# Kernel tuning notes

Measured on AMD Instinct MI355X. Metric: run time of the kernel, lower is better.

Reference implementation:

```python
import jax, jax.numpy as jnp
import numpy as np

N, K = 50000, 16
IN_FEATS, HIDDEN, T2V = 128, 128, 64


def time2vec(t, w0, b0, W, B):
    # t: [..., 1] -> [..., T2V]; linear term + sin periodic terms
    lin = t * w0 + b0                      # [..., 1]
    per = jnp.sin(t * W + B)               # [..., T2V-1]
    return jnp.concatenate([lin, per], axis=-1)


def setup_inputs() -> dict:
    key = jax.random.key(0)
    ks = jax.random.split(key, 12)
    s = 0.05
    return {
        "x": jax.random.normal(ks[0], (N, IN_FEATS), jnp.float32),
        "ts": jax.random.uniform(ks[1], (N, K), jnp.float32),
        "idx": jax.random.randint(ks[2], (N, K), 0, N),
        "t2v_w0": jax.random.normal(ks[3], (1,), jnp.float32),
        "t2v_b0": jax.random.normal(ks[4], (1,), jnp.float32),
        "t2v_W": jax.random.normal(ks[5], (T2V - 1,), jnp.float32),
        "t2v_B": jax.random.normal(ks[6], (T2V - 1,), jnp.float32),
        "Wq": jax.random.normal(ks[7], (IN_FEATS + T2V, HIDDEN), jnp.float32) * s,
        "Wk": jax.random.normal(ks[8], (IN_FEATS + T2V, HIDDEN), jnp.float32) * s,
        "Wv": jax.random.normal(ks[9], (IN_FEATS + T2V, HIDDEN), jnp.float32) * s,
        "Wo": jax.random.normal(ks[10], (HIDDEN, HIDDEN), jnp.float32) * s,
        "bo": jnp.zeros((HIDDEN,), jnp.float32),
    }


def reference(x, ts, idx, t2v_w0, t2v_b0, t2v_W, t2v_B, Wq, Wk, Wv, Wo, bo):
    # Self representation: node feats + time2vec of zero time offset
    te_self = time2vec(jnp.zeros((x.shape[0], 1), x.dtype), t2v_w0, t2v_b0, t2v_W, t2v_B)  # [N, T2V]
    h_self = jnp.concatenate([x, te_self], axis=-1)           # [N, IN+T2V]

    # Neighbor gather + time2vec of interaction times
    x_nbr = x[idx]                                             # [N, K, IN]
    te_nbr = time2vec(ts[..., None], t2v_w0, t2v_b0, t2v_W, t2v_B)  # [N, K, T2V]
    h_nbr = jnp.concatenate([x_nbr, te_nbr], axis=-1)          # [N, K, IN+T2V]

    # Single-head scaled dot-product attention over neighbors
    q = h_self @ Wq                                            # [N, H]
    k = jnp.einsum('nkf,fh->nkh', h_nbr, Wk)                   # [N, K, H]
    v = jnp.einsum('nkf,fh->nkh', h_nbr, Wv)                   # [N, K, H]
    scores = jnp.einsum('nh,nkh->nk', q, k) / jnp.sqrt(jnp.asarray(HIDDEN, x.dtype))
    attn = jax.nn.softmax(scores, axis=-1)                     # [N, K]
    agg = jnp.einsum('nk,nkh->nh', attn, v)                    # [N, H]

    return jax.nn.relu(agg @ Wo + bo)                          # [N, H]
```

## Files before the change

### kernel.cpp

```cpp
#include <hip/hip_runtime.h>
#include <math.h>

#define NN 50000
#define SCL 0.08838834764831845f

#define QX    0
#define QKX   6400000
#define WVOT  9600000
#define WVOB  9616384
#define QC    9624576
#define MQK   9624704
#define CQK   9632896
#define WT    9632960
#define BT    9633024
#define UBASE 9633088
#define KXB   0
#define VOB   6400000
#define WCAT  12800000
#define WVOP  12857344

typedef __attribute__((ext_vector_type(8))) short bf16x8;
typedef __attribute__((ext_vector_type(4))) float f32x4;

__device__ __forceinline__ float bfl(unsigned int u) {
  union { unsigned int i; float f; } v; v.i = u << 16; return v.f;
}
__device__ __forceinline__ float bfh(unsigned int u) {
  union { unsigned int i; float f; } v; v.i = u & 0xffff0000u; return v.f;
}
__device__ __forceinline__ unsigned short f2bf(float f) {
  union { float f; unsigned int i; } v; v.f = f;
  return (unsigned short)((v.i + 0x7fff + ((v.i >> 16) & 1)) >> 16);
}

__global__ __launch_bounds__(128) void tgat_prep(
    const float* __restrict__ Wq, const float* __restrict__ Wk,
    const float* __restrict__ Wv, const float* __restrict__ Wo,
    const float* __restrict__ t2v_b0, const float* __restrict__ t2v_B,
    float* __restrict__ ws) {
  const int h = threadIdx.x;
  const int b = blockIdx.x;
  if (b < 192) {
    const float* wvrow = Wv + b * 128;
    float acc = 0.f;
#pragma unroll 8
    for (int f = 0; f < 128; ++f) acc += wvrow[f] * Wo[f * 128 + h];
    if (b < 128) ws[WVOT + b * 128 + h] = acc;
    else         ws[WVOB + (b - 128) * 128 + h] = acc;
  } else if (b == 192) {
    float acc = t2v_b0[0] * Wq[128 * 128 + h];
    for (int j = 1; j < 64; ++j)
      acc += __sinf(t2v_B[j - 1]) * Wq[(128 + j) * 128 + h];
    ws[QC + h] = acc;
  } else {
    const int f = b - 193;
    if (h < 64) {
      const float* wqrow = Wq + f * 128;
      const float* wkrow = Wk + (128 + h) * 128;
      float acc = 0.f;
#pragma unroll 8
      for (int i = 0; i < 128; ++i) acc += wqrow[i] * wkrow[i];
      ws[MQK + f * 64 + h] = SCL * acc;
    }
  }
}

__global__ __launch_bounds__(128) void tgat_prep2(
    const float* __restrict__ Wq, const float* __restrict__ Wk,
    const float* __restrict__ t2v_w0, const float* __restrict__ t2v_b0,
    const float* __restrict__ t2v_W, const float* __restrict__ t2v_B,
    float* __restrict__ ws, unsigned short* __restrict__ ub) {
  const int t = threadIdx.x, b = blockIdx.x;
  if (b < 448) {
    float v;
    if (b < 128)      v = Wq[t * 128 + b];
    else if (b < 256) v = Wk[t * 128 + (b - 128)];
    else if (b < 384) v = ws[WVOT + t * 128 + (b - 256)];
    else              v = ws[MQK + t * 64 + (b - 384)];
    ub[WCAT + b * 128 + t] = f2bf(v);
  } else if (b == 448) {
    if (t < 64) {
      const float* wkrow = Wk + (128 + t) * 128;
      float acc = 0.f;
#pragma unroll 8
      for (int i = 0; i < 128; ++i) acc += ws[QC + i] * wkrow[i];
      ws[CQK + t] = SCL * acc;
    }
  } else if (b == 449) {
    if (t < 64) {
      ws[WT + t] = (t == 0) ? t2v_w0[0] : t2v_W[t - 1];
      ws[BT + t] = (t == 0) ? t2v_b0[0] : t2v_B[t - 1];
    }
  } else {
    const int j = b - 450;
    if (t < 64) {
      const float lo = ws[WVOB + j * 128 + 2 * t];
      const float hi = ws[WVOB + j * 128 + 2 * t + 1];
      unsigned* wp = (unsigned*)(ub + WVOP);
      wp[j * 64 + t] = (unsigned)f2bf(lo) | ((unsigned)f2bf(hi) << 16);
    }
  }
}

__global__ __launch_bounds__(64) void tgat_precomp_mfma(
    const float* __restrict__ x, const unsigned short* __restrict__ ub,
    float* ws) {
  const int lane = threadIdx.x;
  const int mr = blockIdx.x * 16;
  const unsigned short* wc = ub + WCAT;
  const int arow = lane & 15;
  const int ko = (lane >> 4) * 8;
  const int rbase = (lane >> 4) * 4;

  bf16x8 afr[4];
  {
    const float* xrow = x + (size_t)(mr + arow) * 128;
#pragma unroll
    for (int kk = 0; kk < 4; ++kk) {
      const float4 lo = *(const float4*)(xrow + kk * 32 + ko);
      const float4 hi = *(const float4*)(xrow + kk * 32 + ko + 4);
      bf16x8 f;
      f[0] = (short)f2bf(lo.x); f[1] = (short)f2bf(lo.y);
      f[2] = (short)f2bf(lo.z); f[3] = (short)f2bf(lo.w);
      f[4] = (short)f2bf(hi.x); f[5] = (short)f2bf(hi.y);
      f[6] = (short)f2bf(hi.z); f[7] = (short)f2bf(hi.w);
      afr[kk] = f;
    }
  }

  unsigned short* kxb = (unsigned short*)(ws + UBASE) + KXB;
  unsigned short* vob = (unsigned short*)(ws + UBASE) + VOB;

#pragma unroll 4
  for (int ct = 0; ct < 28; ++ct) {
    const int col = ct * 16 + arow;
    bf16x8 bfr[4];
#pragma unroll
    for (int kk = 0; kk < 4; ++kk)
      bfr[kk] = *(const bf16x8*)(wc + (size_t)col * 128 + kk * 32 + ko);
    f32x4 acc = {0.f, 0.f, 0.f, 0.f};
#pragma unroll
    for (int kk = 0; kk < 4; ++kk)
      acc = __builtin_amdgcn_mfma_f32_16x16x32_bf16(afr[kk], bfr[kk], acc, 0, 0, 0);

    const int gc = ct * 16 + arow;
    if (ct < 8) {
      const float qc = ws[QC + gc];
#pragma unroll
      for (int r = 0; r < 4; ++r)
        ws[QX + (size_t)(mr + rbase + r) * 128 + gc] = (acc[r] + qc) * SCL;
    } else if (ct < 16) {
#pragma unroll
      for (int r = 0; r < 4; ++r)
        kxb[(size_t)(mr + rbase + r) * 128 + (gc - 128)] = f2bf(acc[r]);
    } else if (ct < 24) {
#pragma unroll
      for (int r = 0; r < 4; ++r)
        vob[(size_t)(mr + rbase + r) * 128 + (gc - 256)] = f2bf(acc[r]);
    } else {
      const float cq = ws[CQK + gc - 384];
#pragma unroll
      for (int r = 0; r < 4; ++r)
        ws[QKX + (size_t)(mr + rbase + r) * 64 + (gc - 384)] = acc[r] + cq;
    }
  }
}

__global__ __launch_bounds__(256, 4) void tgat_main(
    const float* __restrict__ ts, const int* __restrict__ idx,
    const float* __restrict__ bo, const float* __restrict__ ws,
    float* __restrict__ out) {
  const int lane = threadIdx.x & 63;
  const int wv   = threadIdx.x >> 6;
  const int my_k = lane >> 2, my_c = lane & 3;

  __shared__ float lds[4 * 1312];
  __shared__ unsigned wvo_l[4096];
  float* te_s = lds + wv * 1312;
  float* s_s  = te_s + 1088;
  float* q_s  = te_s + 1104;
  float* qk_s = te_s + 1248;

  const float* qx  = ws + QX;
  const float* qkx = ws + QKX;
  const unsigned short* ubr = (const unsigned short*)(ws + UBASE);
  const unsigned short* kxb = ubr + KXB;
  const unsigned short* vob = ubr + VOB;

  const int n = blockIdx.x * 4 + wv;

  {
    const uint4* wvp = (const uint4*)(ubr + WVOP);
#pragma unroll
    for (int i = 0; i < 4; ++i)
      ((uint4*)wvo_l)[threadIdx.x + i * 256] = wvp[threadIdx.x + i * 256];
  }

  const int   iv = idx[n * 16 + (lane & 15)];
  const float tv = ts[n * 16 + (lane & 15)];
  const float2 qv = ((const float2*)(qx + (size_t)n * 128))[lane];
  const float qkv = qkx[(size_t)n * 64 + lane];
  const float2 bo2 = ((const float2*)bo)[lane];

  const int i_myk = __shfl(iv, my_k, 64);
  const unsigned short* kr = kxb + (size_t)i_myk * 128 + my_c * 32;
  const uint4 kx0 = *(const uint4*)(kr);
  const uint4 kx1 = *(const uint4*)(kr + 8);
  const uint4 kx2 = *(const uint4*)(kr + 16);
  const uint4 kx3 = *(const uint4*)(kr + 24);
  unsigned int vg[16];
#pragma unroll
  for (int k = 0; k < 16; ++k) {
    const int ik = __shfl(iv, k, 64);
    vg[k] = ((const unsigned int*)(vob + (size_t)ik * 128))[lane];
  }

  const float tvk = __shfl(tv, my_k, 64);
  float te[16];
  {
    const float4* w4 = (const float4*)(ws + WT + my_c * 16);
    const float4* b4 = (const float4*)(ws + BT + my_c * 16);
#pragma unroll
    for (int i4 = 0; i4 < 4; ++i4) {
      const float4 a = w4[i4], b = b4[i4];
      te[i4*4+0] = __sinf(tvk * a.x + b.x);
      te[i4*4+1] = __sinf(tvk * a.y + b.y);
      te[i4*4+2] = __sinf(tvk * a.z + b.z);
      te[i4*4+3] = __sinf(tvk * a.w + b.w);
    }
  }
  if (my_c == 0) te[0] = tvk * (ws[WT]) + ws[BT];

  {
    const int f = 2 * lane;
    const int qi = (f >> 5) * 36 + (f & 31);
    q_s[qi] = qv.x; q_s[qi + 1] = qv.y;
  }
  qk_s[lane] = qkv;
#pragma unroll
  for (int i = 0; i < 16; ++i)
    te_s[(my_c * 16 + i) * 17 + my_k] = te[i];
  asm volatile("s_waitcnt lgkmcnt(0)" ::: "memory");

  float p = 0.f;
  {
    const float4* qb = (const float4*)(q_s + my_c * 36);
#pragma unroll
    for (int q8 = 0; q8 < 4; ++q8) {
      const uint4 u = (q8 == 0) ? kx0 : (q8 == 1) ? kx1 : (q8 == 2) ? kx2 : kx3;
      const float4 qlo = qb[q8 * 2], qhi = qb[q8 * 2 + 1];
      p += bfl(u.x) * qlo.x + bfh(u.x) * qlo.y;
      p += bfl(u.y) * qlo.z + bfh(u.y) * qlo.w;
      p += bfl(u.z) * qhi.x + bfh(u.z) * qhi.y;
      p += bfl(u.w) * qhi.z + bfh(u.w) * qhi.w;
    }
    const float4* qq4 = (const float4*)(qk_s + my_c * 16);
#pragma unroll
    for (int i4 = 0; i4 < 4; ++i4) {
      const float4 q = qq4[i4];
      p += te[i4*4+0]*q.x + te[i4*4+1]*q.y + te[i4*4+2]*q.z + te[i4*4+3]*q.w;
    }
  }
  p += __shfl_xor(p, 1, 64);
  p += __shfl_xor(p, 2, 64);
  if (my_c == 0) s_s[my_k] = p;
  asm volatile("s_waitcnt lgkmcnt(0)" ::: "memory");

  float a[16];
  {
    float sv[16];
    const float4* s4 = (const float4*)s_s;
#pragma unroll
    for (int i4 = 0; i4 < 4; ++i4) {
      const float4 v = s4[i4];
      sv[i4*4+0]=v.x; sv[i4*4+1]=v.y; sv[i4*4+2]=v.z; sv[i4*4+3]=v.w;
    }
    float m = sv[0];
#pragma unroll
    for (int k = 1; k < 16; ++k) m = fmaxf(m, sv[k]);
    float sum = 0.f;
#pragma unroll
    for (int k = 0; k < 16; ++k) { a[k] = __expf(sv[k] - m); sum += a[k]; }
    const float inv = 1.f / sum;
#pragma unroll
    for (int k = 0; k < 16; ++k) a[k] *= inv;
  }

  {
    float ta = 0.f;
#pragma unroll
    for (int k = 0; k < 16; ++k) ta += a[k] * te_s[lane * 17 + k];
    qk_s[lane] = ta;
  }
  asm volatile("s_waitcnt lgkmcnt(0)" ::: "memory");

  float acc0 = bo2.x, acc1 = bo2.y;
#pragma unroll
  for (int k = 0; k < 16; ++k) {
    const unsigned int u = vg[k];
    acc0 += a[k] * bfl(u);
    acc1 += a[k] * bfh(u);
  }

  __syncthreads();
  {
    const float4* ta4 = (const float4*)qk_s;
#pragma unroll
    for (int j4 = 0; j4 < 16; ++j4) {
      const float4 tb = ta4[j4];
      const unsigned u0 = wvo_l[(j4*4+0) * 64 + lane];
      const unsigned u1 = wvo_l[(j4*4+1) * 64 + lane];
      const unsigned u2 = wvo_l[(j4*4+2) * 64 + lane];
      const unsigned u3 = wvo_l[(j4*4+3) * 64 + lane];
      acc0 += tb.x * bfl(u0); acc1 += tb.x * bfh(u0);
      acc0 += tb.y * bfl(u1); acc1 += tb.y * bfh(u1);
      acc0 += tb.z * bfl(u2); acc1 += tb.z * bfh(u2);
      acc0 += tb.w * bfl(u3); acc1 += tb.w * bfh(u3);
    }
  }

  float2 o; o.x = fmaxf(acc0, 0.f); o.y = fmaxf(acc1, 0.f);
  ((float2*)(out + (size_t)n * 128))[lane] = o;
}

extern "C" void kernel_launch(void* const* d_in, const int* in_sizes, int n_in,
                              void* d_out, int out_size, void* d_ws, size_t ws_size,
                              hipStream_t stream) {
  const float* x    = (const float*)d_in[0];
  const float* ts   = (const float*)d_in[1];
  const int*   idx  = (const int*)  d_in[2];
  const float* w0   = (const float*)d_in[3];
  const float* b0   = (const float*)d_in[4];
  const float* t2vW = (const float*)d_in[5];
  const float* t2vB = (const float*)d_in[6];
  const float* Wq   = (const float*)d_in[7];
  const float* Wk   = (const float*)d_in[8];
  const float* Wv   = (const float*)d_in[9];
  const float* Wo   = (const float*)d_in[10];
  const float* bo   = (const float*)d_in[11];
  float* ws = (float*)d_ws;
  unsigned short* ub = (unsigned short*)(ws + UBASE);
  float* out = (float*)d_out;

  tgat_prep<<<321, 128, 0, stream>>>(Wq, Wk, Wv, Wo, b0, t2vB, ws);
  tgat_prep2<<<514, 128, 0, stream>>>(Wq, Wk, w0, b0, t2vW, t2vB, ws, ub);
  tgat_precomp_mfma<<<3125, 64, 0, stream>>>(x, ub, ws);
  tgat_main<<<12500, 256, 0, stream>>>(ts, idx, bo, ws, out);
}
```

Baseline: 218.8 us.

## Store Q and QK projections as bf16 and enlarge precompute MFMA tiles

After: 226.2 us. 1.03x slower.

```diff
diff --git a/kernel.cpp b/kernel.cpp
--- a/kernel.cpp
+++ b/kernel.cpp
@@ -4,20 +4,17 @@
 #define NN 50000
 #define SCL 0.08838834764831845f
 
-#define QX    0
-#define QKX   6400000
-#define WVOT  9600000
-#define WVOB  9616384
-#define QC    9624576
-#define MQK   9624704
-#define CQK   9632896
-#define WT    9632960
-#define BT    9633024
-#define UBASE 9633088
-#define KXB   0
-#define VOB   6400000
-#define WCAT  12800000
-#define WVOP  12857344
+#define QC    0
+#define CQK   128
+#define WT    192
+#define BT    256
+#define UBASE 320
+#define QXB   0
+#define KXB   6400000
+#define VOB   12800000
+#define QKXB  19200000
+#define WCAT  22400000
+#define WVOP  22457344
 
 typedef __attribute__((ext_vector_type(8))) short bf16x8;
 typedef __attribute__((ext_vector_type(4))) float f32x4;
@@ -36,23 +33,38 @@
 __global__ __launch_bounds__(128) void tgat_prep(
     const float* __restrict__ Wq, const float* __restrict__ Wk,
     const float* __restrict__ Wv, const float* __restrict__ Wo,
-    const float* __restrict__ t2v_b0, const float* __restrict__ t2v_B,
-    float* __restrict__ ws) {
+    const float* __restrict__ t2v_w0, const float* __restrict__ t2v_b0,
+    const float* __restrict__ t2v_W, const float* __restrict__ t2v_B,
+    float* __restrict__ ws, unsigned short* __restrict__ ub) {
   const int h = threadIdx.x;
   const int b = blockIdx.x;
-  if (b < 192) {
+  __shared__ float row_s[128];
+
+  if (b < 128) {
     const float* wvrow = Wv + b * 128;
     float acc = 0.f;
 #pragma unroll 8
     for (int f = 0; f < 128; ++f) acc += wvrow[f] * Wo[f * 128 + h];
-    if (b < 128) ws[WVOT + b * 128 + h] = acc;
-    else         ws[WVOB + (b - 128) * 128 + h] = acc;
+    ub[WCAT + (256 + h) * 128 + b] = f2bf(acc);
+  } else if (b < 192) {
+    const int j = b - 128;
+    const float* wvrow = Wv + (128 + j) * 128;
+    float acc = 0.f;
+#pragma unroll 8
+    for (int f = 0; f < 128; ++f) acc += wvrow[f] * Wo[f * 128 + h];
+    row_s[h] = acc;
+    __syncthreads();
+    if (h < 64) {
+      unsigned* wp = (unsigned*)(ub + WVOP);
+      wp[j * 64 + h] = (unsigned)f2bf(row_s[2 * h]) |
+                       ((unsigned)f2bf(row_s[2 * h + 1]) << 16);
+    }
   } else if (b == 192) {
     float acc = t2v_b0[0] * Wq[128 * 128 + h];
     for (int j = 1; j < 64; ++j)
       acc += __sinf(t2v_B[j - 1]) * Wq[(128 + j) * 128 + h];
     ws[QC + h] = acc;
-  } else {
+  } else if (b < 321) {
     const int f = b - 193;
     if (h < 64) {
       const float* wqrow = Wq + f * 128;
@@ -60,61 +72,46 @@
       float acc = 0.f;
 #pragma unroll 8
       for (int i = 0; i < 128; ++i) acc += wqrow[i] * wkrow[i];
-      ws[MQK + f * 64 + h] = SCL * acc;
-    }
-  }
-}
-
-__global__ __launch_bounds__(128) void tgat_prep2(
-    const float* __restrict__ Wq, const float* __restrict__ Wk,
-    const float* __restrict__ t2v_w0, const float* __restrict__ t2v_b0,
-    const float* __restrict__ t2v_W, const float* __restrict__ t2v_B,
-    float* __restrict__ ws, unsigned short* __restrict__ ub) {
-  const int t = threadIdx.x, b = blockIdx.x;
-  if (b < 448) {
-    float v;
-    if (b < 128)      v = Wq[t * 128 + b];
-    else if (b < 256) v = Wk[t * 128 + (b - 128)];
-    else if (b < 384) v = ws[WVOT + t * 128 + (b - 256)];
-    else              v = ws[MQK + t * 64 + (b - 384)];
-    ub[WCAT + b * 128 + t] = f2bf(v);
-  } else if (b == 448) {
-    if (t < 64) {
-      const float* wkrow = Wk + (128 + t) * 128;
-      float acc = 0.f;
+      ub[WCAT + (384 + h) * 128 + f] = f2bf(SCL * acc);
+    }
+  } else if (b < 577) {
+    const int c = b - 321;
+    const float v = (c < 128) ? Wq[h * 128 + c] : Wk[h * 128 + (c - 128)];
+    ub[WCAT + c * 128 + h] = f2bf(v);
+  } else {
+    if (h < 64) {
+      ws[WT + h] = (h == 0) ? t2v_w0[0] : t2v_W[h - 1];
+      ws[BT + h] = (h == 0) ? t2v_b0[0] : t2v_B[h - 1];
+    }
+  }
+}
+
+__global__ __launch_bounds__(64) void tgat_prep2(
+    const float* __restrict__ Wk, float* __restrict__ ws) {
+  const int j = threadIdx.x;
+  const float* wkrow = Wk + (128 + j) * 128;
+  float acc = 0.f;
 #pragma unroll 8
-      for (int i = 0; i < 128; ++i) acc += ws[QC + i] * wkrow[i];
-      ws[CQK + t] = SCL * acc;
-    }
-  } else if (b == 449) {
-    if (t < 64) {
-      ws[WT + t] = (t == 0) ? t2v_w0[0] : t2v_W[t - 1];
-      ws[BT + t] = (t == 0) ? t2v_b0[0] : t2v_B[t - 1];
-    }
-  } else {
-    const int j = b - 450;
-    if (t < 64) {
-      const float lo = ws[WVOB + j * 128 + 2 * t];
-      const float hi = ws[WVOB + j * 128 + 2 * t + 1];
-      unsigned* wp = (unsigned*)(ub + WVOP);
-      wp[j * 64 + t] = (unsigned)f2bf(lo) | ((unsigned)f2bf(hi) << 16);
-    }
-  }
-}
-
-__global__ __launch_bounds__(64) void tgat_precomp_mfma(
-    const float* __restrict__ x, const unsigned short* __restrict__ ub,
-    float* ws) {
-  const int lane = threadIdx.x;
-  const int mr = blockIdx.x * 16;
+  for (int i = 0; i < 128; ++i) acc += ws[QC + i] * wkrow[i];
+  ws[CQK + j] = SCL * acc;
+}
+
+__global__ __launch_bounds__(256, 4) void tgat_precomp_mfma(
+    const float* __restrict__ x, float* ws) {
+  const int lane = threadIdx.x & 63;
+  const int wv = threadIdx.x >> 6;
+  const int mr = blockIdx.x * 128 + wv * 32;
+  unsigned short* ub = (unsigned short*)(ws + UBASE);
   const unsigned short* wc = ub + WCAT;
   const int arow = lane & 15;
   const int ko = (lane >> 4) * 8;
   const int rbase = (lane >> 4) * 4;
 
-  bf16x8 afr[4];
-  {
-    const float* xrow = x + (size_t)(mr + arow) * 128;
+  bf16x8 afr[2][4];
+#pragma unroll
+  for (int tile = 0; tile < 2; ++tile) {
+    const int row = mr + tile * 16 + arow;
+    const float* xrow = x + (size_t)((row < NN) ? row : (NN - 1)) * 128;
 #pragma unroll
     for (int kk = 0; kk < 4; ++kk) {
       const float4 lo = *(const float4*)(xrow + kk * 32 + ko);
@@ -124,44 +121,57 @@
       f[2] = (short)f2bf(lo.z); f[3] = (short)f2bf(lo.w);
       f[4] = (short)f2bf(hi.x); f[5] = (short)f2bf(hi.y);
       f[6] = (short)f2bf(hi.z); f[7] = (short)f2bf(hi.w);
-      afr[kk] = f;
-    }
-  }
-
-  unsigned short* kxb = (unsigned short*)(ws + UBASE) + KXB;
-  unsigned short* vob = (unsigned short*)(ws + UBASE) + VOB;
-
-#pragma unroll 4
+      afr[tile][kk] = f;
+    }
+  }
+
+  unsigned short* qxb  = ub + QXB;
+  unsigned short* kxb  = ub + KXB;
+  unsigned short* vob  = ub + VOB;
+  unsigned short* qkxb = ub + QKXB;
+
+#pragma unroll 2
   for (int ct = 0; ct < 28; ++ct) {
     const int col = ct * 16 + arow;
     bf16x8 bfr[4];
 #pragma unroll
     for (int kk = 0; kk < 4; ++kk)
       bfr[kk] = *(const bf16x8*)(wc + (size_t)col * 128 + kk * 32 + ko);
-    f32x4 acc = {0.f, 0.f, 0.f, 0.f};
-#pragma unroll
-    for (int kk = 0; kk < 4; ++kk)
-      acc = __builtin_amdgcn_mfma_f32_16x16x32_bf16(afr[kk], bfr[kk], acc, 0, 0, 0);
+    f32x4 acc0 = {0.f, 0.f, 0.f, 0.f}, acc1 = {0.f, 0.f, 0.f, 0.f};
+#pragma unroll
+    for (int kk = 0; kk < 4; ++kk) {
+      acc0 = __builtin_amdgcn_mfma_f32_16x16x32_bf16(afr[0][kk], bfr[kk], acc0, 0, 0, 0);
+      acc1 = __builtin_amdgcn_mfma_f32_16x16x32_bf16(afr[1][kk], bfr[kk], acc1, 0, 0, 0);
+    }
 
     const int gc = ct * 16 + arow;
-    if (ct < 8) {
-      const float qc = ws[QC + gc];
-#pragma unroll
-      for (int r = 0; r < 4; ++r)
-        ws[QX + (size_t)(mr + rbase + r) * 128 + gc] = (acc[r] + qc) * SCL;
-    } else if (ct < 16) {
-#pragma unroll
-      for (int r = 0; r < 4; ++r)
-        kxb[(size_t)(mr + rbase + r) * 128 + (gc - 128)] = f2bf(acc[r]);
-    } else if (ct < 24) {
-#pragma unroll
-      for (int r = 0; r < 4; ++r)
-        vob[(size_t)(mr + rbase + r) * 128 + (gc - 256)] = f2bf(acc[r]);
-    } else {
-      const float cq = ws[CQK + gc - 384];
-#pragma unroll
-      for (int r = 0; r < 4; ++r)
-        ws[QKX + (size_t)(mr + rbase + r) * 64 + (gc - 384)] = acc[r] + cq;
+#pragma unroll
+    for (int tile = 0; tile < 2; ++tile) {
+      const f32x4 acc = tile ? acc1 : acc0;
+      const int r0 = mr + tile * 16 + rbase;
+      if (ct < 8) {
+        const float qc = ws[QC + gc];
+#pragma unroll
+        for (int r = 0; r < 4; ++r)
+          if (r0 + r < NN)
+            qxb[(size_t)(r0 + r) * 128 + gc] = f2bf((acc[r] + qc) * SCL);
+      } else if (ct < 16) {
+#pragma unroll
+        for (int r = 0; r < 4; ++r)
+          if (r0 + r < NN)
+            kxb[(size_t)(r0 + r) * 128 + (gc - 128)] = f2bf(acc[r]);
+      } else if (ct < 24) {
+#pragma unroll
+        for (int r = 0; r < 4; ++r)
+          if (r0 + r < NN)
+            vob[(size_t)(r0 + r) * 128 + (gc - 256)] = f2bf(acc[r]);
+      } else {
+        const float cq = ws[CQK + gc - 384];
+#pragma unroll
+        for (int r = 0; r < 4; ++r)
+          if (r0 + r < NN)
+            qkxb[(size_t)(r0 + r) * 64 + (gc - 384)] = f2bf(acc[r] + cq);
+      }
     }
   }
 }
@@ -181,11 +191,11 @@
   float* q_s  = te_s + 1104;
   float* qk_s = te_s + 1248;
 
-  const float* qx  = ws + QX;
-  const float* qkx = ws + QKX;
   const unsigned short* ubr = (const unsigned short*)(ws + UBASE);
-  const unsigned short* kxb = ubr + KXB;
-  const unsigned short* vob = ubr + VOB;
+  const unsigned short* qxb  = ubr + QXB;
+  const unsigned short* kxb  = ubr + KXB;
+  const unsigned short* vob  = ubr + VOB;
+  const unsigned short* qkxb = ubr + QKXB;
 
   const int n = blockIdx.x * 4 + wv;
 
@@ -198,8 +208,9 @@
 
   const int   iv = idx[n * 16 + (lane & 15)];
   const float tv = ts[n * 16 + (lane & 15)];
-  const float2 qv = ((const float2*)(qx + (size_t)n * 128))[lane];
-  const float qkv = qkx[(size_t)n * 64 + lane];
+  const unsigned qu = ((const unsigned*)(qxb + (size_t)n * 128))[lane];
+  unsigned qku = 0;
+  if (lane < 32) qku = ((const unsigned*)(qkxb + (size_t)n * 64))[lane];
   const float2 bo2 = ((const float2*)bo)[lane];
 
   const int i_myk = __shfl(iv, my_k, 64);
@@ -234,9 +245,9 @@
   {
     const int f = 2 * lane;
     const int qi = (f >> 5) * 36 + (f & 31);
-    q_s[qi] = qv.x; q_s[qi + 1] = qv.y;
-  }
-  qk_s[lane] = qkv;
+    q_s[qi] = bfl(qu); q_s[qi + 1] = bfh(qu);
+  }
+  if (lane < 32) { qk_s[2 * lane] = bfl(qku); qk_s[2 * lane + 1] = bfh(qku); }
 #pragma unroll
   for (int i = 0; i < 16; ++i)
     te_s[(my_c * 16 + i) * 17 + my_k] = te[i];
@@ -342,8 +353,8 @@
   unsigned short* ub = (unsigned short*)(ws + UBASE);
   float* out = (float*)d_out;
 
-  tgat_prep<<<321, 128, 0, stream>>>(Wq, Wk, Wv, Wo, b0, t2vB, ws);
-  tgat_prep2<<<514, 128, 0, stream>>>(Wq, Wk, w0, b0, t2vW, t2vB, ws, ub);
-  tgat_precomp_mfma<<<3125, 64, 0, stream>>>(x, ub, ws);
+  tgat_prep<<<578, 128, 0, stream>>>(Wq, Wk, Wv, Wo, w0, b0, t2vW, t2vB, ws, ub);
+  tgat_prep2<<<1, 64, 0, stream>>>(Wk, ws);
+  tgat_precomp_mfma<<<391, 256, 0, stream>>>(x, ws);
   tgat_main<<<12500, 256, 0, stream>>>(ts, idx, bo, ws, out);
 }
```
